# Optimization experiments

Hardware: AMD Instinct MI355X
Metric: run time of the kernel (lower is better)

## Reference

```python
import jax, jax.numpy as jnp
from jax import lax
import numpy as np

B, T, NAG, MTASK = 8, 32, 50, 100  # batch, timesteps, n agents, m tasks
MTOP, NNB, L, H = 10, 10, 5, 512   # M top tasks, N neighbors (must equal M), L, hidden_dim
IN_DIM = NNB * MTOP * L + NNB * MTASK + NNB + NNB * MTOP  # 1610


def setup_inputs() -> dict:
    key = jax.random.key(0)
    ks = jax.random.split(key, 8)
    return {
        "beta": jax.random.normal(ks[0], (B, T, NAG, MTASK, L), dtype=jnp.float32),
        "actions_onehot": jax.random.uniform(ks[1], (B, T, NAG, MTASK), dtype=jnp.float32),
        "power_states": jax.random.normal(ks[2], (B, T, NAG), dtype=jnp.float32),
        "prev_assigns": jax.random.randint(ks[3], (B, T, NAG), 0, MTASK, dtype=jnp.int32),
        "W1": jax.random.normal(ks[4], (IN_DIM, H), dtype=jnp.float32) * 0.02,
        "b1": jnp.zeros((H,), jnp.float32),
        "W2": jax.random.normal(ks[5], (H, H), dtype=jnp.float32) * 0.02,
        "b2": jnp.zeros((H,), jnp.float32),
        "W3": jax.random.normal(ks[6], (H, MTOP + 1), dtype=jnp.float32) * 0.02,
        "b3": jnp.zeros((MTOP + 1,), jnp.float32),
    }


def _gather_agents(x, nb_flat):
    # x: [B,T,n,...]; nb_flat: [B,T,n*N] int -> [B,T,n,N,...]
    idx = nb_flat.reshape(B, T, NAG * NNB, *([1] * (x.ndim - 3)))
    out = jnp.take_along_axis(x, idx, axis=2)
    return out.reshape(B, T, NAG, NNB, *x.shape[3:])


def reference(beta, actions_onehot, power_states, prev_assigns, W1, b1, W2, b2, W3, b3):
    total_beta = beta.sum(-1)                              # [B,T,n,m]
    _, tasks = lax.top_k(total_beta, MTOP)                 # [B,T,n,M] top tasks per agent

    # benefit of agent a's best among agent i's top-M tasks: [B,T,i,a]
    tb_g = jnp.take_along_axis(total_beta, tasks.reshape(B, T, 1, NAG * MTOP), axis=3)
    best = tb_g.reshape(B, T, NAG, NAG, MTOP).max(-1)      # [B,T,a,i]
    best = best.transpose(0, 1, 3, 2)                      # [B,T,i,a]
    best = jnp.where(jnp.eye(NAG, dtype=bool), -jnp.inf, best)
    _, neighbors = lax.top_k(best, NNB)                    # [B,T,n,N]
    nb_flat = neighbors.reshape(B, T, NAG * NNB)

    # beta features: beta[b,t,nb(i,j),tasks(i,k),l] flattened in (M,N,L) order
    beta_nb = _gather_agents(beta, nb_flat)                # [B,T,n,N,m,L]
    beta_sel = jnp.take_along_axis(beta_nb, tasks[:, :, :, None, :, None], axis=4)  # [B,T,n,N,M,L]
    beta_feat = beta_sel.transpose(0, 1, 2, 4, 3, 5).reshape(B, T, NAG, NNB * MTOP * L)

    act_feat = _gather_agents(actions_onehot, nb_flat).reshape(B, T, NAG, NNB * MTASK)
    pow_feat = _gather_agents(power_states, nb_flat)       # [B,T,n,N]

    pa_nb = _gather_agents(prev_assigns, nb_flat)          # [B,T,n,N] int
    # one_hot(prev_assign)[task] == (prev_assign == task); flattened (M,N) order
    prev_feat = (tasks[:, :, :, :, None] == pa_nb[:, :, :, None, :]).astype(beta.dtype)
    prev_feat = prev_feat.reshape(B, T, NAG, MTOP * NNB)

    inputs = jnp.concatenate([beta_feat, act_feat, pow_feat, prev_feat], axis=-1)  # [B,T,n,1610]
    x = jax.nn.relu(inputs @ W1 + b1)
    x = jax.nn.relu(x @ W2 + b2)
    q = x @ W3 + b3                                        # [B,T,n,M+1]
    return q
```

## Files before the change

### kernel.cpp

```cpp
#include <hip/hip_runtime.h>
#include <math.h>

#define NB 8
#define NT 32
#define NAG 50
#define MTASK 100
#define MTOP 10
#define NNB 10
#define LDIM 5
#define HDIM 512
#define INDIM 1610
#define KP1 1664
#define NKT1 (KP1/32)
#define NKT2 (HDIM/32)
#define NROWS (NB*NT*NAG)
#define NOUT (MTOP+1)
#define NTOPKB (NROWS/4)
#define NPREPX (KP1/64 + HDIM/64)
#define NPREPB (NPREPX * (HDIM/64))

typedef float f32x4 __attribute__((ext_vector_type(4)));
typedef _Float16 f16;
typedef _Float16 f16x8 __attribute__((ext_vector_type(8)));

__device__ __forceinline__ void gload16(const void* g, void* l) {
    __builtin_amdgcn_global_load_lds(
        (__attribute__((address_space(1))) void*)(g),
        (__attribute__((address_space(3))) void*)(l), 16, 0, 0);
}


__global__ __launch_bounds__(256) void k_topk_prep(
    const float* __restrict__ beta, float* __restrict__ total_beta,
    int* __restrict__ tasks,
    const float* __restrict__ W1, const float* __restrict__ W2,
    f16* __restrict__ T1, f16* __restrict__ T2) {
    __shared__ float lds[64][65];
    if (blockIdx.x < NTOPKB) {
        int wid = threadIdx.x >> 6, lane = threadIdx.x & 63;
        int row = blockIdx.x * 4 + wid;
        const float* bp = beta + (size_t)row * MTASK * LDIM;
        float v1, v2 = -INFINITY;
        {
            const float* p = bp + lane * LDIM;
            v1 = p[0] + p[1] + p[2] + p[3] + p[4];
            total_beta[(size_t)row * MTASK + lane] = v1;
        }
        if (lane + 64 < MTASK) {
            const float* p = bp + (lane + 64) * LDIM;
            v2 = p[0] + p[1] + p[2] + p[3] + p[4];
            total_beta[(size_t)row * MTASK + lane + 64] = v2;
        }
        for (int k = 0; k < MTOP; ++k) {
            float v; int idx;
            if (v1 >= v2) { v = v1; idx = lane; } else { v = v2; idx = lane + 64; }
            #pragma unroll
            for (int m = 1; m < 64; m <<= 1) {
                float vo = __shfl_xor(v, m, 64);
                int io = __shfl_xor(idx, m, 64);
                if (vo > v || (vo == v && io < idx)) { v = vo; idx = io; }
            }
            if (lane == 0) tasks[row * MTOP + k] = idx;
            if (idx == lane) v1 = -INFINITY;
            else if (idx == lane + 64) v2 = -INFINITY;
        }
    } else {
        int pb = blockIdx.x - NTOPKB;
        int bx = pb % NPREPX, n0 = (pb / NPREPX) * 64;
        const float* W; f16* T; int K, NKT, kp0;
        if (bx < KP1 / 64) { W = W1; T = T1; K = INDIM; NKT = NKT1; kp0 = bx * 64; }
        else               { W = W2; T = T2; K = HDIM;  NKT = NKT2; kp0 = (bx - KP1 / 64) * 64; }
        int t = threadIdx.x;
        int cc = t & 63, r0 = t >> 6;
        #pragma unroll
        for (int i = 0; i < 16; ++i) {
            int rr = r0 + i * 4;
            int kp = kp0 + rr;
            lds[rr][cc] = (kp < K) ? W[(size_t)kp * HDIM + n0 + cc] : 0.f;
        }
        __syncthreads();
        int nblk = n0 >> 6;
        #pragma unroll
        for (int s = 0; s < 2; ++s) {
            int o = t + s * 256;
            int rn = o & 63, ko = o >> 6;
            int kp = kp0 + ko * 8;
            int kt = kp >> 5, kc = (kp >> 3) & 3;
            f16 h8[8];
            #pragma unroll
            for (int e = 0; e < 8; ++e) h8[e] = (f16)lds[ko * 8 + e][rn];
            size_t off = ((size_t)(nblk * NKT + kt) * 4 + kc) * 512 + rn * 8;
            *(f16x8*)&T[off] = *(f16x8*)h8;
        }
    }
}

__global__ __launch_bounds__(256) void k_nbrs(const float* __restrict__ total_beta,
                                              const int* __restrict__ tasks,
                                              int* __restrict__ neighbors) {
    int wid = threadIdx.x >> 6, lane = threadIdx.x & 63;
    int row = blockIdx.x * 4 + wid;
    int bt = row / NAG, i = row - bt * NAG;
    int tk[MTOP];
    #pragma unroll
    for (int k = 0; k < MTOP; ++k) tk[k] = tasks[row * MTOP + k];
    float v1 = -INFINITY;
    if (lane < NAG) {
        const float* tba = total_beta + ((size_t)bt * NAG + lane) * MTASK;
        float mx = -INFINITY;
        #pragma unroll
        for (int k = 0; k < MTOP; ++k) mx = fmaxf(mx, tba[tk[k]]);
        v1 = (lane == i) ? -INFINITY : mx;
    }
    for (int k = 0; k < NNB; ++k) {
        float v = v1; int idx = lane;
        #pragma unroll
        for (int m = 1; m < 64; m <<= 1) {
            float vo = __shfl_xor(v, m, 64);
            int io = __shfl_xor(idx, m, 64);
            if (vo > v || (vo == v && io < idx)) { v = vo; idx = io; }
        }
        if (lane == 0) neighbors[row * NNB + k] = idx;
        if (idx == lane) v1 = -INFINITY;
    }
}

__global__ __launch_bounds__(256) void k_build_inputs(
    const float* __restrict__ beta, const float* __restrict__ actions,
    const float* __restrict__ power, const int* __restrict__ prev,
    const int* __restrict__ tasks, const int* __restrict__ neighbors,
    f16* __restrict__ A) {
    int b = blockIdx.x;
    int t = threadIdx.x;
    __shared__ int tkv[8][MTOP], nbv[8][NNB], pav[8][NNB];
    __shared__ float pwv[8][NNB];
    __shared__ float fbuf[8][500];
    __shared__ float abuf[8][1004];
    if (t < 80) {
        int lr = t / 10, j = t - lr * 10;
        int row = b * 8 + lr;
        int bt = row / NAG;
        int nbj = neighbors[row * NNB + j];
        nbv[lr][j] = nbj;
        pav[lr][j] = prev[bt * NAG + nbj];
        pwv[lr][j] = power[bt * NAG + nbj];
        tkv[lr][j] = tasks[row * MTOP + j];
    }
    __syncthreads();
    int row0 = b * 8;
    #pragma unroll
    for (int it = 0; it < 4; ++it) {
        int idx = t + it * 256;
        if (idx < 800) {
            int l = idx / 100, p = idx - l * 100;
            int k = p / 10, j = p - k * 10;
            int row = row0 + l;
            int bt = row / NAG;
            const float* src = beta + ((size_t)(bt * NAG + nbv[l][j]) * MTASK
                                       + tkv[l][k]) * LDIM;
            int c0 = k * 50 + j * 5;
            #pragma unroll
            for (int i = 0; i < 5; ++i) fbuf[l][c0 + i] = src[i];
        }
    }
    #pragma unroll
    for (int it = 0; it < 8; ++it) {
        int idx = t + it * 256;
        if (idx < 2000) {
            int l = idx / 250, v = idx - l * 250;
            int j = v / 25, q = v - j * 25;
            int row = row0 + l;
            int bt = row / NAG;
            f32x4 a = *(const f32x4*)&actions[(size_t)(bt * NAG + nbv[l][j]) * MTASK + q * 4];
            *(f32x4*)&abuf[l][j * 100 + q * 4] = a;
        }
    }
    __syncthreads();
    int l = t & 7, og = t >> 3;
    int row = row0 + l;
    int rb = row >> 6, rlo = row & 63;
    #pragma unroll
    for (int s = 0; s < 7; ++s) {
        int o = og + 32 * s;
        if (o < 208) {
            f16 h8[8];
            #pragma unroll
            for (int e = 0; e < 8; ++e) {
                int c = o * 8 + e;
                float f;
                if (c < 500) {
                    f = fbuf[l][c];
                } else if (c < 1500) {
                    f = abuf[l][c - 500];
                } else if (c < 1510) {
                    f = pwv[l][c - 1500];
                } else if (c < 1610) {
                    int r2 = c - 1510, k = r2 / NNB, j = r2 - k * NNB;
                    f = (tkv[l][k] == pav[l][j]) ? 1.f : 0.f;
                } else {
                    f = 0.f;
                }
                h8[e] = (f16)f;
            }
            size_t off = ((size_t)rb * 208 + o) * 512 + rlo * 8;
            *(f16x8*)&A[off] = *(f16x8*)h8;
        }
    }
}

template<int NKT, int MODE>
__global__ __launch_bounds__(256, 4) void k_gemm(
    const f16* __restrict__ Ap, const f16* __restrict__ Bp,
    const float* __restrict__ bias, f16* __restrict__ C,
    const float* __restrict__ W3, float* __restrict__ qpart) {
    constexpr int SMEM = (MODE == 0) ? 34048 : 39680;
    __shared__ __align__(16) char smem[SMEM];
    f16* sB = (f16*)smem;
    int tid = threadIdx.x, wid = tid >> 6, lane = tid & 63;
    int id = blockIdx.x;
    int swz = (id & 7) * 100 + (id >> 3);
    int nt = swz & 3, mt = swz >> 2;

    auto stage = [&](int kk, int buf) {
        #pragma unroll
        for (int j = 0; j < 2; ++j) {
            int seg = wid + 4 * j;
            int q = seg >> 2, kc = seg & 3;
            gload16(Bp + ((size_t)((2 * nt + q) * NKT + kk) * 4 + kc) * 512 + lane * 8,
                    sB + buf * 4096 + (kc * 128 + q * 64) * 8);
        }
    };

    int wr = wid >> 1, wc = wid & 1;
    int lrow = lane & 15, lk = lane >> 4;
    f32x4 acc[2][4] = {};

    stage(0, 0);
    for (int kk = 0; kk < NKT; ++kk) {
        int buf = kk & 1;
        __syncthreads();
        size_t abase = ((size_t)(mt * NKT + kk) * 4 + lk) * 512 + (wr * 32 + lrow) * 8;
        f16x8 a0 = *(const f16x8*)(Ap + abase);
        f16x8 a1 = *(const f16x8*)(Ap + abase + 128);
        if (kk + 1 < NKT) stage(kk + 1, buf ^ 1);
        f16x8 bh[4];
        #pragma unroll
        for (int j = 0; j < 4; ++j)
            bh[j] = *(const f16x8*)(sB + buf * 4096 + (lk * 128 + wc * 64 + j * 16 + lrow) * 8);
        #pragma unroll
        for (int j = 0; j < 4; ++j) {
            acc[0][j] = __builtin_amdgcn_mfma_f32_16x16x32_f16(a0, bh[j], acc[0][j], 0, 0, 0);
            acc[1][j] = __builtin_amdgcn_mfma_f32_16x16x32_f16(a1, bh[j], acc[1][j], 0, 0, 0);
        }
    }

    __syncthreads();
    float* sE = (float*)smem;
    #pragma unroll
    for (int i = 0; i < 2; ++i)
        #pragma unroll
        for (int j = 0; j < 4; ++j)
            #pragma unroll
            for (int r = 0; r < 4; ++r)
                sE[(wr * 32 + i * 16 + lk * 4 + r) * 133 + wc * 64 + j * 16 + lrow] = acc[i][j][r];

    if constexpr (MODE == 0) {
        __syncthreads();
        int l2 = tid & 63, og2 = tid >> 6;
        #pragma unroll
        for (int s2 = 0; s2 < 4; ++s2) {
            int o = og2 + 4 * s2;
            int n0 = nt * 128 + o * 8;
            f32x4 v0 = *(f32x4*)&sE[l2 * 133 + o * 8];
            f32x4 v1 = *(f32x4*)&sE[l2 * 133 + o * 8 + 4];
            f32x4 bb0 = *(const f32x4*)&bias[n0];
            f32x4 bb1 = *(const f32x4*)&bias[n0 + 4];
            f16 h8[8];
            #pragma unroll
            for (int i = 0; i < 4; ++i) {
                h8[i] = (f16)fmaxf(v0[i] + bb0[i], 0.f);
                h8[4 + i] = (f16)fmaxf(v1[i] + bb1[i], 0.f);
            }
            size_t off = ((size_t)mt * 64 + nt * 16 + o) * 512 + l2 * 8;
            *(f16x8*)&C[off] = *(f16x8*)h8;
        }
    } else {
        float* W3s = (float*)(smem + 34048);
        for (int i = tid; i < 128 * NOUT; i += 256)
            W3s[i] = W3[nt * 128 * NOUT + i];
        __syncthreads();
        int row = tid >> 2, seg = tid & 3;
        float a11[NOUT];
        #pragma unroll
        for (int n = 0; n < NOUT; ++n) a11[n] = 0.f;
        #pragma unroll
        for (int c32 = 0; c32 < 32; ++c32) {
            int col = seg + 4 * c32;
            float h = fmaxf(sE[row * 133 + col] + bias[nt * 128 + col], 0.f);
            const float* w = W3s + col * NOUT;
            #pragma unroll
            for (int n = 0; n < NOUT; ++n) a11[n] += h * w[n];
        }
        #pragma unroll
        for (int d = 2; d >= 1; d >>= 1)
            #pragma unroll
            for (int n = 0; n < NOUT; ++n) a11[n] += __shfl_down(a11[n], d, 64);
        if (seg == 0) {
            int grow = mt * 64 + row;
            #pragma unroll
            for (int n = 0; n < NOUT; ++n)
                qpart[(size_t)nt * NROWS * NOUT + (size_t)grow * NOUT + n] = a11[n];
        }
    }
}

__global__ __launch_bounds__(256) void k_qreduce(const float* __restrict__ qp,
                                                 const float* __restrict__ b3,
                                                 float* __restrict__ out) {
    int i = blockIdx.x * 256 + threadIdx.x;
    if (i < NROWS * NOUT) {
        int n = i % NOUT;
        const size_t P = (size_t)NROWS * NOUT;
        out[i] = b3[n] + qp[i] + qp[i + P] + qp[i + 2 * P] + qp[i + 3 * P];
    }
}

extern "C" void kernel_launch(void* const* d_in, const int* in_sizes, int n_in,
                              void* d_out, int out_size, void* d_ws, size_t ws_size,
                              hipStream_t stream) {
    const float* beta    = (const float*)d_in[0];
    const float* actions = (const float*)d_in[1];
    const float* power   = (const float*)d_in[2];
    const int*   prev    = (const int*)d_in[3];
    const float* W1      = (const float*)d_in[4];
    const float* b1      = (const float*)d_in[5];
    const float* W2      = (const float*)d_in[6];
    const float* b2      = (const float*)d_in[7];
    const float* W3      = (const float*)d_in[8];
    const float* b3      = (const float*)d_in[9];
    float* out = (float*)d_out;

    char* ws = (char*)d_ws;
    size_t off = 0;
    auto alloc = [&](size_t bytes) { void* p = ws + off; off += (bytes + 255) & ~(size_t)255; return p; };
    float* total_beta = (float*)alloc((size_t)NROWS * MTASK * 4);
    int*   tasks      = (int*)  alloc((size_t)NROWS * MTOP * 4);
    int*   neighbors  = (int*)  alloc((size_t)NROWS * NNB * 4);
    f16*   A    = (f16*)alloc((size_t)NROWS * KP1 * 2);
    f16*   W1t  = (f16*)alloc((size_t)HDIM * KP1 * 2);
    f16*   W2t  = (f16*)alloc((size_t)HDIM * HDIM * 2);
    f16*   h1   = (f16*)alloc((size_t)NROWS * HDIM * 2);
    float* qpart = (float*)alloc((size_t)4 * NROWS * NOUT * 4);

    k_topk_prep<<<NTOPKB + NPREPB, 256, 0, stream>>>(beta, total_beta, tasks,
                                                     W1, W2, W1t, W2t);
    k_nbrs<<<NROWS / 4, 256, 0, stream>>>(total_beta, tasks, neighbors);
    k_build_inputs<<<NROWS / 8, 256, 0, stream>>>(beta, actions, power, prev, tasks,
                                                  neighbors, A);
    k_gemm<NKT1, 0><<<800, 256, 0, stream>>>(A, W1t, b1, h1, nullptr, nullptr);
    k_gemm<NKT2, 1><<<800, 256, 0, stream>>>(h1, W2t, b2, nullptr, W3, qpart);
    k_qreduce<<<(NROWS * NOUT + 255) / 256, 256, 0, stream>>>(qpart, b3, out);
}
```

Baseline: 141.8 us.

## Triple-buffer B tiles in LDS and register-prefetch A fragments in GEMM loop

The GEMM main loop goes from double to triple buffering of the B tile in shared memory, issuing loads two k-steps ahead. A barrier guarded by an explicit vmcnt wait replaces the plain __syncthreads. The A-operand fragments are now loaded one iteration ahead into registers, so MFMA work overlaps global-memory latency instead of stalling on it. This costs extra LDS for the third buffer and more vector registers, and it depends on manual waitcnt bookkeeping being correct.

```diff
diff --git a/kernel.cpp b/kernel.cpp
--- a/kernel.cpp
+++ b/kernel.cpp
@@ -235,23 +235,36 @@
     int lrow = lane & 15, lk = lane >> 4;
     f32x4 acc[2][4] = {};
 
+    auto aaddr = [&](int kk) {
+        return ((size_t)(mt * NKT + kk) * 4 + lk) * 512 + (wr * 32 + lrow) * 8;
+    };
+
     stage(0, 0);
+    size_t ab0 = aaddr(0);
+    f16x8 aCur0 = *(const f16x8*)(Ap + ab0);
+    f16x8 aCur1 = *(const f16x8*)(Ap + ab0 + 128);
+    stage(1, 1);
     for (int kk = 0; kk < NKT; ++kk) {
-        int buf = kk & 1;
-        __syncthreads();
-        size_t abase = ((size_t)(mt * NKT + kk) * 4 + lk) * 512 + (wr * 32 + lrow) * 8;
-        f16x8 a0 = *(const f16x8*)(Ap + abase);
-        f16x8 a1 = *(const f16x8*)(Ap + abase + 128);
-        if (kk + 1 < NKT) stage(kk + 1, buf ^ 1);
+        asm volatile("s_waitcnt vmcnt(2)" ::: "memory");
+        __builtin_amdgcn_s_barrier();
+        __builtin_amdgcn_sched_barrier(0);
+        if (kk + 2 < NKT) stage(kk + 2, (kk + 2) % 3);
+        int kn = (kk + 1 < NKT) ? kk + 1 : kk;
+        size_t abn = aaddr(kn);
+        f16x8 aN0 = *(const f16x8*)(Ap + abn);
+        f16x8 aN1 = *(const f16x8*)(Ap + abn + 128);
+        const f16* bb = sB + (kk % 3) * 4096;
         f16x8 bh[4];
         #pragma unroll
         for (int j = 0; j < 4; ++j)
-            bh[j] = *(const f16x8*)(sB + buf * 4096 + (lk * 128 + wc * 64 + j * 16 + lrow) * 8);
+            bh[j] = *(const f16x8*)(bb + (lk * 128 + wc * 64 + j * 16 + lrow) * 8);
         #pragma unroll
         for (int j = 0; j < 4; ++j) {
-            acc[0][j] = __builtin_amdgcn_mfma_f32_16x16x32_f16(a0, bh[j], acc[0][j], 0, 0, 0);
-            acc[1][j] = __builtin_amdgcn_mfma_f32_16x16x32_f16(a1, bh[j], acc[1][j], 0, 0, 0);
-        }
+            acc[0][j] = __builtin_amdgcn_mfma_f32_16x16x32_f16(aCur0, bh[j], acc[0][j], 0, 0, 0);
+            acc[1][j] = __builtin_amdgcn_mfma_f32_16x16x32_f16(aCur1, bh[j], acc[1][j], 0, 0, 0);
+        }
+        aCur0 = aN0;
+        aCur1 = aN1;
     }
 
     __syncthreads();
```

Result: no change. 142.0 us (+0.2%).
